# Kernel tuning notes

Measured on AMD Instinct MI355X. Metric: run time of the kernel, lower is better.

Reference implementation:

```python
import jax, jax.numpy as jnp
import numpy as np

B, Lq, Lkv = 4, 1024, 4096
Cq, Ckv, E, NH = 512, 512, 512, 8
HD = E // NH


def setup_inputs() -> dict:
    key = jax.random.key(0)
    ks = jax.random.split(key, 8)
    s = 0.02
    return {
        "Xq": jax.random.normal(ks[0], (B, Lq, Cq), dtype=jnp.float32),
        "Xkv": jax.random.normal(ks[1], (B, Lkv, Ckv), dtype=jnp.float32),
        "mask": jax.random.randint(ks[2], (B, Lq, 1), 0, 2, dtype=jnp.int32),
        "Wq": jax.random.normal(ks[3], (Cq, E), dtype=jnp.float32) * s,
        "bq": jnp.zeros((E,), dtype=jnp.float32),
        "Wkv": jax.random.normal(ks[4], (Ckv, 2 * E), dtype=jnp.float32) * s,
        "bkv": jnp.zeros((2 * E,), dtype=jnp.float32),
        "Wp": jax.random.normal(ks[5], (E, E), dtype=jnp.float32) * s,
        "bp": jnp.zeros((E,), dtype=jnp.float32),
        "attn_pos": jax.random.normal(ks[6], (1, NH, Lq, Lkv), dtype=jnp.float32) * s,
    }


def reference(Xq, Xkv, mask, Wq, bq, Wkv, bkv, Wp, bp, attn_pos):
    scale = HD ** -0.5
    # projections
    Q = (Xq @ Wq + bq).reshape(B, Lq, NH, HD).transpose(0, 2, 1, 3) * scale  # [B,NH,Lq,HD]
    KV = (Xkv @ Wkv + bkv).reshape(B, Lkv, 2, NH, HD)
    K = KV[:, :, 0].transpose(0, 2, 1, 3)  # [B,NH,Lkv,HD]
    V = KV[:, :, 1].transpose(0, 2, 1, 3)
    # scores + learned positional bias
    attn = jnp.einsum('bhqd,bhkd->bhqk', Q, K) + attn_pos  # [B,NH,Lq,Lkv]
    # dummy-column masked softmax (mask: [B,Lq,1], 1=keep row)
    m = mask.astype(attn.dtype)[:, None]           # [B,1,Lq,1]
    attn = attn + (1.0 - m) * (-100.0)             # suppress masked query rows
    dummy = jnp.broadcast_to(jnp.where(m == 0, 100.0, -100.0), (B, NH, Lq, 1))
    attn = jax.nn.softmax(jnp.concatenate([attn, dummy], axis=-1), axis=-1)[..., :Lkv]
    # weighted sum + output projection (dropout = identity in eval)
    out = jnp.einsum('bhqk,bhkd->bhqd', attn, V)
    out = out.transpose(0, 2, 1, 3).reshape(B, Lq, E)
    return out @ Wp + bp
```

## Files before the change

### kernel.cpp

```cpp
#include <hip/hip_runtime.h>

typedef unsigned short u16;
typedef __attribute__((ext_vector_type(8))) short bf16x8;
typedef __attribute__((ext_vector_type(4))) float f32x4;
typedef __attribute__((ext_vector_type(2))) unsigned u32x2;
typedef __attribute__((ext_vector_type(4))) unsigned u32x4;

__device__ __forceinline__ u16 f2bf(float x) {
    union { float f; unsigned u; } v; v.f = x;
    unsigned r = v.u + 0x7FFF + ((v.u >> 16) & 1);
    return (u16)(r >> 16);
}

__device__ __forceinline__ unsigned cvt_pk_bf16(float lo, float hi) {
    unsigned r;
    asm("v_cvt_pk_bf16_f32 %0, %1, %2" : "=v"(r) : "v"(lo), "v"(hi));
    return r;
}

__device__ __forceinline__ bf16x8 pk8(const f32x4& s0, const f32x4& s1) {
    union { u32x4 u; bf16x8 v; } x;
    x.u[0] = cvt_pk_bf16(s0[0], s0[1]);
    x.u[1] = cvt_pk_bf16(s0[2], s0[3]);
    x.u[2] = cvt_pk_bf16(s1[0], s1[1]);
    x.u[3] = cvt_pk_bf16(s1[2], s1[3]);
    return x.v;
}

__device__ __forceinline__ void gl_lds16(const u16* g, u16* l) {
    __builtin_amdgcn_global_load_lds((const __attribute__((address_space(1))) void*)g,
                                     (__attribute__((address_space(3))) void*)l, 16, 0, 0);
}

__global__ __launch_bounds__(256) void conv_bf16(const float* __restrict__ in,
                                                 u16* __restrict__ out) {
    size_t i = ((size_t)blockIdx.x * 256 + threadIdx.x) * 8;
    const float4* p = (const float4*)(in + i);
    float4 a = p[0], b = p[1];
    u32x4 w = {cvt_pk_bf16(a.x, a.y), cvt_pk_bf16(a.z, a.w),
               cvt_pk_bf16(b.x, b.y), cvt_pk_bf16(b.z, b.w)};
    *(u32x4*)(out + i) = w;
}

__global__ __launch_bounds__(256) void transpose_w(const float* __restrict__ in,
                                                   u16* __restrict__ out, int R, int C) {
    __shared__ float tile[64][65];
    int r0 = blockIdx.y * 64, c0 = blockIdx.x * 64;
    int tid = threadIdx.x;
#pragma unroll
    for (int j = 0; j < 16; ++j) {
        int e = tid + j * 256;
        int row = e >> 6, col = e & 63;
        tile[row][col] = in[(size_t)(r0 + row) * C + c0 + col];
    }
    __syncthreads();
#pragma unroll
    for (int j = 0; j < 16; ++j) {
        int e = tid + j * 256;
        int row = e >> 6, col = e & 63;
        out[(size_t)(c0 + row) * R + r0 + col] = f2bf(tile[col][row]);
    }
}

__global__ __launch_bounds__(256) void transpose_v(const u16* __restrict__ in,
                                                   u16* __restrict__ out) {
    __shared__ u16 tile[64][65];
    int bh = blockIdx.y;
    int r0 = blockIdx.x * 64;
    const u16* ip = in + (size_t)bh * 4096 * 64;
    u16* op = out + (size_t)bh * 64 * 4096;
    int tid = threadIdx.x;
#pragma unroll
    for (int j = 0; j < 16; ++j) {
        int e = tid + j * 256;
        int row = e >> 6, col = e & 63;
        tile[row][col] = ip[(size_t)(r0 + row) * 64 + col];
    }
    __syncthreads();
#pragma unroll
    for (int j = 0; j < 16; ++j) {
        int e = tid + j * 256;
        int row = e >> 6, col = e & 63;
        int c5 = col & 31;
        int src = (col & 32) | ((((c5 >> 2) & 1) << 4) + ((c5 >> 3) << 2) + (c5 & 3));
        op[(size_t)row * 4096 + r0 + col] = tile[src][row];
    }
}

template <int MODE>
__global__ __launch_bounds__(256) void gemm_kernel(const u16* __restrict__ A,
                                                   const u16* __restrict__ Bt,
                                                   const float* __restrict__ bias,
                                                   void* __restrict__ Cout,
                                                   void* __restrict__ Cout2,
                                                   int M, int N, int K) {
    __shared__ u16 Al[128][64];
    __shared__ u16 Bl[128][64];
    int tid = threadIdx.x;
    int lane = tid & 63, wid = tid >> 6;
    int wr = wid >> 1, wc = wid & 1;
    int l15 = lane & 15, g = lane >> 4;
    int bm = blockIdx.y, bn = blockIdx.x;
    int ldr = lane >> 3, ldc = (lane & 7) << 3;

    f32x4 acc[4][4];
#pragma unroll
    for (int m = 0; m < 4; ++m)
#pragma unroll
        for (int n = 0; n < 4; ++n)
#pragma unroll
            for (int j = 0; j < 4; ++j) acc[m][n][j] = 0.f;

    int nK = K >> 6;
    for (int kt = 0; kt < nK; ++kt) {
        __syncthreads();
#pragma unroll
        for (int i = 0; i < 4; ++i) {
            int c = wid * 4 + i;
            int row = c * 8 + ldr;
            gl_lds16(A + (size_t)(bm * 128 + row) * K + kt * 64 + ldc, &Al[0][0] + c * 512);
            gl_lds16(Bt + (size_t)(bn * 128 + row) * K + kt * 64 + ldc, &Bl[0][0] + c * 512);
        }
        __syncthreads();

#pragma unroll
        for (int kk = 0; kk < 2; ++kk) {
            bf16x8 af[4], bfr[4];
#pragma unroll
            for (int m = 0; m < 4; ++m)
                af[m] = *(const bf16x8*)&Al[wr * 64 + m * 16 + l15][kk * 32 + g * 8];
#pragma unroll
            for (int n = 0; n < 4; ++n)
                bfr[n] = *(const bf16x8*)&Bl[wc * 64 + n * 16 + l15][kk * 32 + g * 8];
#pragma unroll
            for (int m = 0; m < 4; ++m)
#pragma unroll
                for (int n = 0; n < 4; ++n)
                    acc[m][n] =
                        __builtin_amdgcn_mfma_f32_16x16x32_bf16(af[m], bfr[n], acc[m][n], 0, 0, 0);
        }
    }

#pragma unroll
    for (int m = 0; m < 4; ++m)
#pragma unroll
        for (int n = 0; n < 4; ++n)
#pragma unroll
            for (int j = 0; j < 4; ++j) {
                int row = bm * 128 + wr * 64 + m * 16 + g * 4 + j;
                int col = bn * 128 + wc * 64 + n * 16 + l15;
                float v = acc[m][n][j] + bias[col];
                if (MODE == 0) {
                    int b = row >> 10, q = row & 1023, h = col >> 6, d = col & 63;
                    ((u16*)Cout)[(((size_t)((b * 8 + h) * 1024 + q)) << 6) + d] =
                        f2bf(v * 0.18033688011112042f);
                } else if (MODE == 1) {
                    int b = row >> 12, kv = row & 4095;
                    int d = col & 63;
                    if (col < 512) {
                        int h = col >> 6;
                        ((u16*)Cout)[(((size_t)((b * 8 + h) * 4096 + kv)) << 6) + d] = f2bf(v);
                    } else {
                        int h = (col - 512) >> 6;
                        ((u16*)Cout2)[(((size_t)((b * 8 + h) * 4096 + kv)) << 6) + d] = f2bf(v);
                    }
                } else {
                    ((float*)Cout)[(size_t)row * N + col] = v;
                }
            }
}

__global__ __launch_bounds__(256, 2) void attn_kernel(const u16* __restrict__ Qb,
                                                      const u16* __restrict__ Kb,
                                                      const u16* __restrict__ Vt,
                                                      const float* __restrict__ pos,
                                                      float* __restrict__ Opart,
                                                      float* __restrict__ Lp) {
    __shared__ u16 Klds[4][4096];
    __shared__ u16 Vlds[4][4096];

    int idx = blockIdx.x;
    int h = idx & 7;
    int rest = idx >> 3;
    int qt = rest & 15, sp = rest >> 4;
    int q0 = qt * 64;
    int kvbase = sp * 1024;
    int tid = threadIdx.x, lane = tid & 63, wid = tid >> 6;
    int l15 = lane & 15, g = lane >> 4;

    bf16x8 aq[4][2];
#pragma unroll
    for (int b = 0; b < 4; ++b) {
        const u16* qp =
            Qb + (((size_t)((b * 8 + h) * 1024 + q0 + wid * 16 + l15)) << 6) + g * 8;
        aq[b][0] = *(const bf16x8*)(qp);
        aq[b][1] = *(const bf16x8*)(qp + 32);
    }

    f32x4 o[4][4];
    f32x4 lacc[4];
#pragma unroll
    for (int b = 0; b < 4; ++b) {
#pragma unroll
        for (int j = 0; j < 4; ++j) lacc[b][j] = 0.f;
#pragma unroll
        for (int n = 0; n < 4; ++n)
#pragma unroll
            for (int j = 0; j < 4; ++j) o[b][n][j] = 0.f;
    }

    const u16* Kg = Kb + ((size_t)(wid * 8 + h)) * 4096 * 64;
    const u16* Vg = Vt + ((size_t)(wid * 8 + h)) * 4096 * 64;
    u16* KldsW = &Klds[wid][0];
    u16* VldsW = &Vlds[wid][0];
    int lr = lane >> 3;
    int lcs = ((lane & 7) ^ lr) << 3;

    const float* posq =
        pos + (size_t)h * 1024 * 4096 + (size_t)(q0 + wid * 16 + l15) * 4096 + kvbase;

    const short one_s = (short)0x3F80;
    bf16x8 ones = {one_s, one_s, one_s, one_s, one_s, one_s, one_s, one_s};
    int sw = (l15 & 7) << 4;

    f32x4 zr[4];
    for (int kt = 0; kt < 16; ++kt) {
        int kv0 = kvbase + kt * 64;
        __syncthreads();
#pragma unroll
        for (int c = 0; c < 8; ++c)
            gl_lds16(Kg + (size_t)(kv0 + c * 8 + lr) * 64 + lcs, KldsW + c * 512);
#pragma unroll
        for (int c = 0; c < 8; ++c)
            gl_lds16(Vg + (size_t)(c * 8 + lr) * 4096 + kv0 + lcs, VldsW + c * 512);
#pragma unroll
        for (int n = 0; n < 4; ++n) {
            zr[n] = *(const f32x4*)(posq + kt * 64 + n * 16 + g * 4);
#pragma unroll
            for (int j = 0; j < 4; ++j) zr[n][j] *= 1.44269504f;
        }
        __syncthreads();

#pragma unroll
        for (int b = 0; b < 4; ++b) {
            const char* KbL = (const char*)&Klds[b][0];
            const char* VbL = (const char*)&Vlds[b][0];

            f32x4 s[4];
            __builtin_amdgcn_s_setprio(1);
#pragma unroll
            for (int n = 0; n < 4; ++n) {
                bf16x8 kb0 = *(const bf16x8*)(KbL + (n * 16 + l15) * 128 + ((g * 16) ^ sw));
                bf16x8 kb1 = *(const bf16x8*)(KbL + (n * 16 + l15) * 128 + ((64 + g * 16) ^ sw));
                f32x4 t = __builtin_amdgcn_mfma_f32_16x16x32_bf16(kb0, aq[b][0], zr[n], 0, 0, 0);
                s[n] = __builtin_amdgcn_mfma_f32_16x16x32_bf16(kb1, aq[b][1], t, 0, 0, 0);
            }
            __builtin_amdgcn_s_setprio(0);

#pragma unroll
            for (int n = 0; n < 4; ++n)
#pragma unroll
                for (int j = 0; j < 4; ++j)
                    s[n][j] = __builtin_exp2f(fminf(s[n][j], 80.f));

            bf16x8 pa0 = pk8(s[0], s[1]);
            bf16x8 pa1 = pk8(s[2], s[3]);

            __builtin_amdgcn_s_setprio(1);
#pragma unroll
            for (int n = 0; n < 4; ++n) {
                bf16x8 vb0 = *(const bf16x8*)(VbL + (n * 16 + l15) * 128 + ((g * 16) ^ sw));
                bf16x8 vb1 = *(const bf16x8*)(VbL + (n * 16 + l15) * 128 + ((64 + g * 16) ^ sw));
                o[b][n] = __builtin_amdgcn_mfma_f32_16x16x32_bf16(pa0, vb0, o[b][n], 0, 0, 0);
                o[b][n] = __builtin_amdgcn_mfma_f32_16x16x32_bf16(pa1, vb1, o[b][n], 0, 0, 0);
            }
            lacc[b] = __builtin_amdgcn_mfma_f32_16x16x32_bf16(pa0, ones, lacc[b], 0, 0, 0);
            lacc[b] = __builtin_amdgcn_mfma_f32_16x16x32_bf16(pa1, ones, lacc[b], 0, 0, 0);
            __builtin_amdgcn_s_setprio(0);
        }
    }

#pragma unroll
    for (int b = 0; b < 4; ++b) {
        int obase = (sp * 32 + b * 8 + h) * 1024;
#pragma unroll
        for (int j = 0; j < 4; ++j) {
            int row = q0 + wid * 16 + g * 4 + j;
#pragma unroll
            for (int n = 0; n < 4; ++n)
                __builtin_nontemporal_store(o[b][n][j],
                                            &Opart[((size_t)(obase + row)) * 64 + n * 16 + l15]);
            if (l15 == 0) __builtin_nontemporal_store(lacc[b][j], &Lp[obase + row]);
        }
    }
}

__global__ __launch_bounds__(256) void attn_combine(const float* __restrict__ Opart,
                                                    const float* __restrict__ Lp,
                                                    const int* __restrict__ mask,
                                                    u16* __restrict__ AO) {
    int tid = threadIdx.x;
    int d = tid & 63;
    int r = blockIdx.x * 4 + (tid >> 6);
    int bh = r >> 10, q = r & 1023;
    int b = bh >> 3, h = bh & 7;

    float L = 0.f, val = 0.f;
#pragma unroll
    for (int s2 = 0; s2 < 4; ++s2) {
        size_t rr = (size_t)(s2 * 32 + bh) * 1024 + q;
        L += Lp[rr];
        val += Opart[rr * 64 + d];
    }
    float res = mask[b * 1024 + q] ? (val / L) : 0.f;
    AO[((size_t)(b * 1024 + q)) * 512 + h * 64 + d] = f2bf(res);
}

extern "C" void kernel_launch(void* const* d_in, const int* in_sizes, int n_in,
                              void* d_out, int out_size, void* d_ws, size_t ws_size,
                              hipStream_t stream) {
    const float* Xq = (const float*)d_in[0];
    const float* Xkv = (const float*)d_in[1];
    const int* mask = (const int*)d_in[2];
    const float* Wq = (const float*)d_in[3];
    const float* bq = (const float*)d_in[4];
    const float* Wkv = (const float*)d_in[5];
    const float* bkv = (const float*)d_in[6];
    const float* Wp = (const float*)d_in[7];
    const float* bp = (const float*)d_in[8];
    const float* pos = (const float*)d_in[9];
    float* out = (float*)d_out;

    char* ws = (char*)d_ws;
    u16* WqT = (u16*)(ws);
    u16* WkvT = (u16*)(ws + 524288);
    u16* WpT = (u16*)(ws + 1572864);
    u16* Qb = (u16*)(ws + 2097152);
    u16* Kb = (u16*)(ws + 6291456);
    u16* Vt = (u16*)(ws + 23068672);
    u16* AO = (u16*)(ws + 39845888);
    float* Opart = (float*)(ws + 44040192);
    u16* Xkvb = (u16*)(ws + 44040192);
    u16* Vtm = (u16*)(ws + 60817408);
    u16* Xqb = (u16*)(ws + 77594624);
    float* Lp = (float*)(ws + 111149056);

    conv_bf16<<<dim3(1024), 256, 0, stream>>>(Xq, Xqb);
    conv_bf16<<<dim3(4096), 256, 0, stream>>>(Xkv, Xkvb);
    transpose_w<<<dim3(8, 8), 256, 0, stream>>>(Wq, WqT, 512, 512);
    transpose_w<<<dim3(16, 8), 256, 0, stream>>>(Wkv, WkvT, 512, 1024);
    transpose_w<<<dim3(8, 8), 256, 0, stream>>>(Wp, WpT, 512, 512);
    gemm_kernel<0><<<dim3(4, 32), 256, 0, stream>>>(Xqb, WqT, bq, Qb, nullptr, 4096, 512, 512);
    gemm_kernel<1><<<dim3(8, 128), 256, 0, stream>>>(Xkvb, WkvT, bkv, Kb, Vtm, 16384, 1024, 512);
    transpose_v<<<dim3(64, 32), 256, 0, stream>>>(Vtm, Vt);
    attn_kernel<<<dim3(512), 256, 0, stream>>>(Qb, Kb, Vt, pos, Opart, Lp);
    attn_combine<<<dim3(8192), 256, 0, stream>>>(Opart, Lp, mask, AO);
    gemm_kernel<2><<<dim3(4, 32), 256, 0, stream>>>(AO, WpT, bp, out, nullptr, 4096, 512, 512);
}
```

Baseline: 186.0 us.

## Split KV into 8 chunks with 32-wide tiles, double occupancy, merge prep kernels

The attention kernel now splits the KV range into 8 partitions of 512 instead of 4 of 1024. It processes 32-column KV tiles with half the LDS, launches 1024 blocks, and raises launch bounds to 4 blocks per CU. The V tile LDS layout and swizzle are reworked so one MFMA per output n-block consumes the 32-wide tile. The clamp before exp2 is dropped, and the combine kernel sums 8 partials. The two bf16 conversions and the three weight transposes are each merged into a single launch to cut launch overhead. The trade-off is more partial-output traffic in the combine, a larger Opart/Lp footprint in the workspace, and possible overflow now that the clamp is gone.

After: 239.3 us. 1.29x slower.

```diff
diff --git a/kernel.cpp b/kernel.cpp
--- a/kernel.cpp
+++ b/kernel.cpp
@@ -32,9 +32,21 @@
                                      (__attribute__((address_space(3))) void*)l, 16, 0, 0);
 }
 
-__global__ __launch_bounds__(256) void conv_bf16(const float* __restrict__ in,
-                                                 u16* __restrict__ out) {
-    size_t i = ((size_t)blockIdx.x * 256 + threadIdx.x) * 8;
+__global__ __launch_bounds__(256) void conv_bf16_2(const float* __restrict__ Xq,
+                                                   const float* __restrict__ Xkv,
+                                                   u16* __restrict__ oq,
+                                                   u16* __restrict__ okv) {
+    int bid = blockIdx.x;
+    const float* in;
+    u16* out;
+    size_t i;
+    if (bid < 1024) {
+        in = Xq; out = oq;
+        i = ((size_t)bid * 256 + threadIdx.x) * 8;
+    } else {
+        in = Xkv; out = okv;
+        i = ((size_t)(bid - 1024) * 256 + threadIdx.x) * 8;
+    }
     const float4* p = (const float4*)(in + i);
     float4 a = p[0], b = p[1];
     u32x4 w = {cvt_pk_bf16(a.x, a.y), cvt_pk_bf16(a.z, a.w),
@@ -42,10 +54,27 @@
     *(u32x4*)(out + i) = w;
 }
 
-__global__ __launch_bounds__(256) void transpose_w(const float* __restrict__ in,
-                                                   u16* __restrict__ out, int R, int C) {
+__global__ __launch_bounds__(256) void transpose_w3(const float* __restrict__ Wq,
+                                                    const float* __restrict__ Wkv,
+                                                    const float* __restrict__ Wp,
+                                                    u16* __restrict__ WqT,
+                                                    u16* __restrict__ WkvT,
+                                                    u16* __restrict__ WpT) {
     __shared__ float tile[64][65];
-    int r0 = blockIdx.y * 64, c0 = blockIdx.x * 64;
+    int bid = blockIdx.x;
+    const float* in;
+    u16* out;
+    int R = 512, C, bx, by;
+    if (bid < 64) {
+        in = Wq; out = WqT; C = 512; bx = bid & 7; by = bid >> 3;
+    } else if (bid < 192) {
+        bid -= 64;
+        in = Wkv; out = WkvT; C = 1024; bx = bid & 15; by = bid >> 4;
+    } else {
+        bid -= 192;
+        in = Wp; out = WpT; C = 512; bx = bid & 7; by = bid >> 3;
+    }
+    int r0 = by * 64, c0 = bx * 64;
     int tid = threadIdx.x;
 #pragma unroll
     for (int j = 0; j < 16; ++j) {
@@ -170,21 +199,21 @@
             }
 }
 
-__global__ __launch_bounds__(256, 2) void attn_kernel(const u16* __restrict__ Qb,
+__global__ __launch_bounds__(256, 4) void attn_kernel(const u16* __restrict__ Qb,
                                                       const u16* __restrict__ Kb,
                                                       const u16* __restrict__ Vt,
                                                       const float* __restrict__ pos,
                                                       float* __restrict__ Opart,
                                                       float* __restrict__ Lp) {
-    __shared__ u16 Klds[4][4096];
-    __shared__ u16 Vlds[4][4096];
+    __shared__ u16 Klds[4][2048];
+    __shared__ u16 Vlds[4][2048];
 
     int idx = blockIdx.x;
     int h = idx & 7;
     int rest = idx >> 3;
     int qt = rest & 15, sp = rest >> 4;
     int q0 = qt * 64;
-    int kvbase = sp * 1024;
+    int kvbase = sp * 512;
     int tid = threadIdx.x, lane = tid & 63, wid = tid >> 6;
     int l15 = lane & 15, g = lane >> 4;
 
@@ -215,6 +244,9 @@
     u16* VldsW = &Vlds[wid][0];
     int lr = lane >> 3;
     int lcs = ((lane & 7) ^ lr) << 3;
+    int vhalf = (lane >> 2) & 1;
+    int vslot = (lane & 3) ^ ((lane >> 3) & 3);
+    int vrow = lane >> 3;
 
     const float* posq =
         pos + (size_t)h * 1024 * 4096 + (size_t)(q0 + wid * 16 + l15) * 4096 + kvbase;
@@ -223,19 +255,20 @@
     bf16x8 ones = {one_s, one_s, one_s, one_s, one_s, one_s, one_s, one_s};
     int sw = (l15 & 7) << 4;
 
-    f32x4 zr[4];
+    f32x4 zr[2];
     for (int kt = 0; kt < 16; ++kt) {
-        int kv0 = kvbase + kt * 64;
+        int kv0 = kvbase + kt * 32;
         __syncthreads();
 #pragma unroll
-        for (int c = 0; c < 8; ++c)
+        for (int c = 0; c < 4; ++c)
             gl_lds16(Kg + (size_t)(kv0 + c * 8 + lr) * 64 + lcs, KldsW + c * 512);
 #pragma unroll
-        for (int c = 0; c < 8; ++c)
-            gl_lds16(Vg + (size_t)(c * 8 + lr) * 4096 + kv0 + lcs, VldsW + c * 512);
-#pragma unroll
-        for (int n = 0; n < 4; ++n) {
-            zr[n] = *(const f32x4*)(posq + kt * 64 + n * 16 + g * 4);
+        for (int c = 0; c < 4; ++c)
+            gl_lds16(Vg + (size_t)(2 * (c * 8 + vrow) + vhalf) * 4096 + kv0 + vslot * 8,
+                     VldsW + c * 512);
+#pragma unroll
+        for (int n = 0; n < 2; ++n) {
+            zr[n] = *(const f32x4*)(posq + kt * 32 + n * 16 + g * 4);
 #pragma unroll
             for (int j = 0; j < 4; ++j) zr[n][j] *= 1.44269504f;
         }
@@ -246,10 +279,10 @@
             const char* KbL = (const char*)&Klds[b][0];
             const char* VbL = (const char*)&Vlds[b][0];
 
-            f32x4 s[4];
+            f32x4 s[2];
             __builtin_amdgcn_s_setprio(1);
 #pragma unroll
-            for (int n = 0; n < 4; ++n) {
+            for (int n = 0; n < 2; ++n) {
                 bf16x8 kb0 = *(const bf16x8*)(KbL + (n * 16 + l15) * 128 + ((g * 16) ^ sw));
                 bf16x8 kb1 = *(const bf16x8*)(KbL + (n * 16 + l15) * 128 + ((64 + g * 16) ^ sw));
                 f32x4 t = __builtin_amdgcn_mfma_f32_16x16x32_bf16(kb0, aq[b][0], zr[n], 0, 0, 0);
@@ -258,24 +291,22 @@
             __builtin_amdgcn_s_setprio(0);
 
 #pragma unroll
-            for (int n = 0; n < 4; ++n)
-#pragma unroll
-                for (int j = 0; j < 4; ++j)
-                    s[n][j] = __builtin_exp2f(fminf(s[n][j], 80.f));
-
-            bf16x8 pa0 = pk8(s[0], s[1]);
-            bf16x8 pa1 = pk8(s[2], s[3]);
+            for (int n = 0; n < 2; ++n)
+#pragma unroll
+                for (int j = 0; j < 4; ++j) s[n][j] = __builtin_exp2f(s[n][j]);
+
+            bf16x8 pa = pk8(s[0], s[1]);
 
             __builtin_amdgcn_s_setprio(1);
 #pragma unroll
             for (int n = 0; n < 4; ++n) {
-                bf16x8 vb0 = *(const bf16x8*)(VbL + (n * 16 + l15) * 128 + ((g * 16) ^ sw));
-                bf16x8 vb1 = *(const bf16x8*)(VbL + (n * 16 + l15) * 128 + ((64 + g * 16) ^ sw));
-                o[b][n] = __builtin_amdgcn_mfma_f32_16x16x32_bf16(pa0, vb0, o[b][n], 0, 0, 0);
-                o[b][n] = __builtin_amdgcn_mfma_f32_16x16x32_bf16(pa1, vb1, o[b][n], 0, 0, 0);
+                int vd = n * 16 + l15;
+                int vr = vd >> 1;
+                int vbyte = (vr << 7) + ((vd & 1) << 6) + (((g ^ (vr & 3)) & 3) << 4);
+                bf16x8 vb = *(const bf16x8*)(VbL + vbyte);
+                o[b][n] = __builtin_amdgcn_mfma_f32_16x16x32_bf16(pa, vb, o[b][n], 0, 0, 0);
             }
-            lacc[b] = __builtin_amdgcn_mfma_f32_16x16x32_bf16(pa0, ones, lacc[b], 0, 0, 0);
-            lacc[b] = __builtin_amdgcn_mfma_f32_16x16x32_bf16(pa1, ones, lacc[b], 0, 0, 0);
+            lacc[b] = __builtin_amdgcn_mfma_f32_16x16x32_bf16(pa, ones, lacc[b], 0, 0, 0);
             __builtin_amdgcn_s_setprio(0);
         }
     }
@@ -307,7 +338,7 @@
 
     float L = 0.f, val = 0.f;
 #pragma unroll
-    for (int s2 = 0; s2 < 4; ++s2) {
+    for (int s2 = 0; s2 < 8; ++s2) {
         size_t rr = (size_t)(s2 * 32 + bh) * 1024 + q;
         L += Lp[rr];
         val += Opart[rr * 64 + d];
@@ -345,15 +376,12 @@
     u16* Xqb = (u16*)(ws + 77594624);
     float* Lp = (float*)(ws + 111149056);
 
-    conv_bf16<<<dim3(1024), 256, 0, stream>>>(Xq, Xqb);
-    conv_bf16<<<dim3(4096), 256, 0, stream>>>(Xkv, Xkvb);
-    transpose_w<<<dim3(8, 8), 256, 0, stream>>>(Wq, WqT, 512, 512);
-    transpose_w<<<dim3(16, 8), 256, 0, stream>>>(Wkv, WkvT, 512, 1024);
-    transpose_w<<<dim3(8, 8), 256, 0, stream>>>(Wp, WpT, 512, 512);
+    conv_bf16_2<<<dim3(5120), 256, 0, stream>>>(Xq, Xkv, Xqb, Xkvb);
+    transpose_w3<<<dim3(256), 256, 0, stream>>>(Wq, Wkv, Wp, WqT, WkvT, WpT);
     gemm_kernel<0><<<dim3(4, 32), 256, 0, stream>>>(Xqb, WqT, bq, Qb, nullptr, 4096, 512, 512);
     gemm_kernel<1><<<dim3(8, 128), 256, 0, stream>>>(Xkvb, WkvT, bkv, Kb, Vtm, 16384, 1024, 512);
     transpose_v<<<dim3(64, 32), 256, 0, stream>>>(Vtm, Vt);
-    attn_kernel<<<dim3(512), 256, 0, stream>>>(Qb, Kb, Vt, pos, Opart, Lp);
+    attn_kernel<<<dim3(1024), 256, 0, stream>>>(Qb, Kb, Vt, pos, Opart, Lp);
     attn_combine<<<dim3(8192), 256, 0, stream>>>(Opart, Lp, mask, AO);
     gemm_kernel<2><<<dim3(4, 32), 256, 0, stream>>>(AO, WpT, bp, out, nullptr, 4096, 512, 512);
 }
```

## Fuse V transpose into KV GEMM epilogue and merge prep kernel launches

Applied to the files above, without the earlier changes.

The KV projection GEMM now writes V directly in the transposed, permuted layout the attention kernel expects, removing the separate transpose_v pass and its intermediate buffer. The input conversions and the three weight transposes are each merged into single launches to cut launch overhead. The exp2 clamp in attention is dropped to save ALU work, at the risk of overflow if scores grow large. The transposed epilogue store is strided and may coalesce poorly.

After: 185.6 us. No clear change (-0.2%).

```diff
diff --git a/kernel.cpp b/kernel.cpp
--- a/kernel.cpp
+++ b/kernel.cpp
@@ -32,9 +32,21 @@
                                      (__attribute__((address_space(3))) void*)l, 16, 0, 0);
 }
 
-__global__ __launch_bounds__(256) void conv_bf16(const float* __restrict__ in,
-                                                 u16* __restrict__ out) {
-    size_t i = ((size_t)blockIdx.x * 256 + threadIdx.x) * 8;
+__global__ __launch_bounds__(256) void conv_bf16_2(const float* __restrict__ Xq,
+                                                   const float* __restrict__ Xkv,
+                                                   u16* __restrict__ oq,
+                                                   u16* __restrict__ okv) {
+    int bid = blockIdx.x;
+    const float* in;
+    u16* out;
+    size_t i;
+    if (bid < 1024) {
+        in = Xq; out = oq;
+        i = ((size_t)bid * 256 + threadIdx.x) * 8;
+    } else {
+        in = Xkv; out = okv;
+        i = ((size_t)(bid - 1024) * 256 + threadIdx.x) * 8;
+    }
     const float4* p = (const float4*)(in + i);
     float4 a = p[0], b = p[1];
     u32x4 w = {cvt_pk_bf16(a.x, a.y), cvt_pk_bf16(a.z, a.w),
@@ -42,10 +54,27 @@
     *(u32x4*)(out + i) = w;
 }
 
-__global__ __launch_bounds__(256) void transpose_w(const float* __restrict__ in,
-                                                   u16* __restrict__ out, int R, int C) {
+__global__ __launch_bounds__(256) void transpose_w3(const float* __restrict__ Wq,
+                                                    const float* __restrict__ Wkv,
+                                                    const float* __restrict__ Wp,
+                                                    u16* __restrict__ WqT,
+                                                    u16* __restrict__ WkvT,
+                                                    u16* __restrict__ WpT) {
     __shared__ float tile[64][65];
-    int r0 = blockIdx.y * 64, c0 = blockIdx.x * 64;
+    int bid = blockIdx.x;
+    const float* in;
+    u16* out;
+    int R = 512, C, bx, by;
+    if (bid < 64) {
+        in = Wq; out = WqT; C = 512; bx = bid & 7; by = bid >> 3;
+    } else if (bid < 192) {
+        bid -= 64;
+        in = Wkv; out = WkvT; C = 1024; bx = bid & 15; by = bid >> 4;
+    } else {
+        bid -= 192;
+        in = Wp; out = WpT; C = 512; bx = bid & 7; by = bid >> 3;
+    }
+    int r0 = by * 64, c0 = bx * 64;
     int tid = threadIdx.x;
 #pragma unroll
     for (int j = 0; j < 16; ++j) {
@@ -59,31 +88,6 @@
         int e = tid + j * 256;
         int row = e >> 6, col = e & 63;
         out[(size_t)(c0 + row) * R + r0 + col] = f2bf(tile[col][row]);
-    }
-}
-
-__global__ __launch_bounds__(256) void transpose_v(const u16* __restrict__ in,
-                                                   u16* __restrict__ out) {
-    __shared__ u16 tile[64][65];
-    int bh = blockIdx.y;
-    int r0 = blockIdx.x * 64;
-    const u16* ip = in + (size_t)bh * 4096 * 64;
-    u16* op = out + (size_t)bh * 64 * 4096;
-    int tid = threadIdx.x;
-#pragma unroll
-    for (int j = 0; j < 16; ++j) {
-        int e = tid + j * 256;
-        int row = e >> 6, col = e & 63;
-        tile[row][col] = ip[(size_t)(r0 + row) * 64 + col];
-    }
-    __syncthreads();
-#pragma unroll
-    for (int j = 0; j < 16; ++j) {
-        int e = tid + j * 256;
-        int row = e >> 6, col = e & 63;
-        int c5 = col & 31;
-        int src = (col & 32) | ((((c5 >> 2) & 1) << 4) + ((c5 >> 3) << 2) + (c5 & 3));
-        op[(size_t)row * 4096 + r0 + col] = tile[src][row];
     }
 }
 
@@ -156,13 +160,15 @@
                         f2bf(v * 0.18033688011112042f);
                 } else if (MODE == 1) {
                     int b = row >> 12, kv = row & 4095;
-                    int d = col & 63;
                     if (col < 512) {
-                        int h = col >> 6;
+                        int h = col >> 6, d = col & 63;
                         ((u16*)Cout)[(((size_t)((b * 8 + h) * 4096 + kv)) << 6) + d] = f2bf(v);
                     } else {
-                        int h = (col - 512) >> 6;
-                        ((u16*)Cout2)[(((size_t)((b * 8 + h) * 4096 + kv)) << 6) + d] = f2bf(v);
+                        int c2 = col - 512;
+                        int h = c2 >> 6, d = c2 & 63;
+                        int p = j | ((m & 1) << 2) | (g << 3);
+                        int dkv = (kv & ~31) | p;
+                        ((u16*)Cout2)[((size_t)(b * 8 + h) * 64 + d) * 4096 + dkv] = f2bf(v);
                     }
                 } else {
                     ((float*)Cout)[(size_t)row * N + col] = v;
@@ -260,8 +266,7 @@
 #pragma unroll
             for (int n = 0; n < 4; ++n)
 #pragma unroll
-                for (int j = 0; j < 4; ++j)
-                    s[n][j] = __builtin_exp2f(fminf(s[n][j], 80.f));
+                for (int j = 0; j < 4; ++j) s[n][j] = __builtin_exp2f(s[n][j]);
 
             bf16x8 pa0 = pk8(s[0], s[1]);
             bf16x8 pa1 = pk8(s[2], s[3]);
@@ -341,18 +346,13 @@
     u16* AO = (u16*)(ws + 39845888);
     float* Opart = (float*)(ws + 44040192);
     u16* Xkvb = (u16*)(ws + 44040192);
-    u16* Vtm = (u16*)(ws + 60817408);
-    u16* Xqb = (u16*)(ws + 77594624);
+    u16* Xqb = (u16*)(ws + 60817408);
     float* Lp = (float*)(ws + 111149056);
 
-    conv_bf16<<<dim3(1024), 256, 0, stream>>>(Xq, Xqb);
-    conv_bf16<<<dim3(4096), 256, 0, stream>>>(Xkv, Xkvb);
-    transpose_w<<<dim3(8, 8), 256, 0, stream>>>(Wq, WqT, 512, 512);
-    transpose_w<<<dim3(16, 8), 256, 0, stream>>>(Wkv, WkvT, 512, 1024);
-    transpose_w<<<dim3(8, 8), 256, 0, stream>>>(Wp, WpT, 512, 512);
+    conv_bf16_2<<<dim3(5120), 256, 0, stream>>>(Xq, Xkv, Xqb, Xkvb);
+    transpose_w3<<<dim3(256), 256, 0, stream>>>(Wq, Wkv, Wp, WqT, WkvT, WpT);
     gemm_kernel<0><<<dim3(4, 32), 256, 0, stream>>>(Xqb, WqT, bq, Qb, nullptr, 4096, 512, 512);
-    gemm_kernel<1><<<dim3(8, 128), 256, 0, stream>>>(Xkvb, WkvT, bkv, Kb, Vtm, 16384, 1024, 512);
-    transpose_v<<<dim3(64, 32), 256, 0, stream>>>(Vtm, Vt);
+    gemm_kernel<1><<<dim3(8, 128), 256, 0, stream>>>(Xkvb, WkvT, bkv, Kb, Vt, 16384, 1024, 512);
     attn_kernel<<<dim3(512), 256, 0, stream>>>(Qb, Kb, Vt, pos, Opart, Lp);
     attn_combine<<<dim3(8192), 256, 0, stream>>>(Opart, Lp, mask, AO);
     gemm_kernel<2><<<dim3(4, 32), 256, 0, stream>>>(AO, WpT, bp, out, nullptr, 4096, 512, 512);
```
